# Kernel tuning notes

Hardware: AMD Instinct MI355X
Metric: run time of the kernel (lower is better)

The kernel has to match this reference:

```python
import jax, jax.numpy as jnp
import numpy as np

N_NODES = 100000
N_EDGES = 1600000
MSG_DIM = 16
HID_DIM = 16
N_ETYPE = 16
N_CLASSES = 64


def setup_inputs() -> dict:
    key = jax.random.key(0)
    ks = jax.random.split(key, 11)
    s = 1.0 / np.sqrt(HID_DIM)
    return {
        "features": jax.random.normal(ks[0], (N_NODES, HID_DIM), dtype=jnp.float32),
        "src": jax.random.randint(ks[1], (N_EDGES,), 0, N_NODES, dtype=jnp.int32),
        "dst": jax.random.randint(ks[2], (N_EDGES,), 0, N_NODES, dtype=jnp.int32),
        "e_type": jax.random.randint(ks[3], (N_EDGES,), 0, N_ETYPE, dtype=jnp.int32),
        "edge_emb": jax.random.normal(ks[4], (N_ETYPE, MSG_DIM * HID_DIM), dtype=jnp.float32),
        "W_ih": jax.random.uniform(ks[5], (3 * HID_DIM, MSG_DIM), dtype=jnp.float32, minval=-s, maxval=s),
        "W_hh": jax.random.uniform(ks[6], (3 * HID_DIM, HID_DIM), dtype=jnp.float32, minval=-s, maxval=s),
        "b_ih": jax.random.uniform(ks[7], (3 * HID_DIM,), dtype=jnp.float32, minval=-s, maxval=s),
        "b_hh": jax.random.uniform(ks[8], (3 * HID_DIM,), dtype=jnp.float32, minval=-s, maxval=s),
        "W_out": jax.random.normal(ks[9], (N_CLASSES, HID_DIM), dtype=jnp.float32) * s,
        "b_out": jax.random.normal(ks[10], (N_CLASSES,), dtype=jnp.float32) * 0.01,
    }


def reference(features, src, dst, e_type, edge_emb, W_ih, W_hh, b_ih, b_hh, W_out, b_out):
    # Per-edge message: A_e @ h_src, A_e = edge-type embedding reshaped [msg, hid]
    A = edge_emb[e_type].reshape(-1, MSG_DIM, HID_DIM)          # [E, M, H]
    msg = jnp.einsum("emh,eh->em", A, features[src])            # [E, M]
    # Sum-aggregate messages into destination nodes
    m = jax.ops.segment_sum(msg, dst, num_segments=N_NODES)     # [N, M]
    # Single-step GRU (PyTorch gate order: r, z, n)
    gx = m @ W_ih.T + b_ih                                      # [N, 3H]
    gh = features @ W_hh.T + b_hh                               # [N, 3H]
    xr, xz, xn = jnp.split(gx, 3, axis=-1)
    hr, hz, hn = jnp.split(gh, 3, axis=-1)
    r = jax.nn.sigmoid(xr + hr)
    z = jax.nn.sigmoid(xz + hz)
    n = jnp.tanh(xn + r * hn)
    h = (1.0 - z) * n + z * features                            # [N, H]
    return h @ W_out.T + b_out                                  # [N, C]
```

## Files before the change

### kernel.cpp

```cpp
#include <hip/hip_runtime.h>

#define NNODES 100000
#define NEDGES 1600000
#define HID 16
#define MSG 16
#define NTYPE 16
#define NCLS 64

__device__ __forceinline__ float sigmoid_f(float x) {
    return 1.0f / (1.0f + __expf(-x));
}

__device__ __forceinline__ float tanh_f(float x) {
    x = fminf(fmaxf(x, -15.0f), 15.0f);
    float e = __expf(2.0f * x);
    return (e - 1.0f) / (e + 1.0f);
}

__global__ __launch_bounds__(256) void ggnn_edge(
    const float* __restrict__ feat,
    const int* __restrict__ src,
    const int* __restrict__ dst,
    const int* __restrict__ etype,
    const float* __restrict__ edge_emb,
    float* __restrict__ magg)
{
    __shared__ float At[NTYPE * MSG * HID];
    for (int idx = threadIdx.x; idx < NTYPE * MSG * HID; idx += 256) {
        int t   = idx >> 8;
        int rem = idx & 255;
        int i   = rem >> 4;
        int hh  = rem & 15;
        At[(t << 8) | (hh << 4) | i] = edge_emb[idx];
    }
    __syncthreads();

    const long long total = (long long)NEDGES * MSG;
    for (long long w = (long long)blockIdx.x * 256 + threadIdx.x; w < total;
         w += (long long)gridDim.x * 256) {
        const int e = (int)(w >> 4);
        const int i = (int)(w & 15);
        const int s = src[e];
        const int d = dst[e];
        const int t = etype[e];

        const float4* fp = (const float4*)(feat + (size_t)s * HID);
        const float4 f0 = fp[0];
        const float4 f1 = fp[1];
        const float4 f2 = fp[2];
        const float4 f3 = fp[3];

        const float* a = At + (t << 8) + i;
        float acc;
        acc  = a[0*16]*f0.x + a[1*16]*f0.y + a[2*16]*f0.z + a[3*16]*f0.w;
        acc += a[4*16]*f1.x + a[5*16]*f1.y + a[6*16]*f1.z + a[7*16]*f1.w;
        acc += a[8*16]*f2.x + a[9*16]*f2.y + a[10*16]*f2.z + a[11*16]*f2.w;
        acc += a[12*16]*f3.x + a[13*16]*f3.y + a[14*16]*f3.z + a[15*16]*f3.w;

        atomicAdd(magg + (size_t)d * MSG + i, acc);
    }
}

__global__ __launch_bounds__(256) void ggnn_node(
    const float* __restrict__ feat,
    const float* __restrict__ magg,
    const float* __restrict__ W_ih,
    const float* __restrict__ W_hh,
    const float* __restrict__ b_ih,
    const float* __restrict__ b_hh,
    const float* __restrict__ W_out,
    const float* __restrict__ b_out,
    float* __restrict__ out)
{
    const int n = blockIdx.x * 256 + threadIdx.x;
    if (n >= NNODES) return;

    float hv[HID], mv[MSG];
    {
        const float4* hp = (const float4*)(feat + (size_t)n * HID);
        const float4* mp = (const float4*)(magg + (size_t)n * MSG);
        #pragma unroll
        for (int q = 0; q < 4; q++) {
            float4 a = hp[q];
            hv[4*q+0] = a.x; hv[4*q+1] = a.y; hv[4*q+2] = a.z; hv[4*q+3] = a.w;
            float4 b = mp[q];
            mv[4*q+0] = b.x; mv[4*q+1] = b.y; mv[4*q+2] = b.z; mv[4*q+3] = b.w;
        }
    }

    float hnew[HID];
    #pragma unroll
    for (int i = 0; i < HID; i++) {
        float xr = b_ih[i], xz = b_ih[16 + i], xn = b_ih[32 + i];
        float hr = b_hh[i], hz = b_hh[16 + i], hn = b_hh[32 + i];
        #pragma unroll
        for (int j = 0; j < HID; j++) {
            xr += W_ih[(i)      * 16 + j] * mv[j];
            xz += W_ih[(16 + i) * 16 + j] * mv[j];
            xn += W_ih[(32 + i) * 16 + j] * mv[j];
            hr += W_hh[(i)      * 16 + j] * hv[j];
            hz += W_hh[(16 + i) * 16 + j] * hv[j];
            hn += W_hh[(32 + i) * 16 + j] * hv[j];
        }
        float r  = sigmoid_f(xr + hr);
        float z  = sigmoid_f(xz + hz);
        float nn = tanh_f(xn + r * hn);
        hnew[i] = (1.0f - z) * nn + z * hv[i];
    }

    float4* op = (float4*)(out + (size_t)n * NCLS);
    #pragma unroll
    for (int c4 = 0; c4 < NCLS / 4; c4++) {
        float a0 = b_out[4*c4+0], a1 = b_out[4*c4+1], a2 = b_out[4*c4+2], a3 = b_out[4*c4+3];
        #pragma unroll
        for (int j = 0; j < HID; j++) {
            a0 += W_out[(4*c4+0) * 16 + j] * hnew[j];
            a1 += W_out[(4*c4+1) * 16 + j] * hnew[j];
            a2 += W_out[(4*c4+2) * 16 + j] * hnew[j];
            a3 += W_out[(4*c4+3) * 16 + j] * hnew[j];
        }
        float4 o; o.x = a0; o.y = a1; o.z = a2; o.w = a3;
        op[c4] = o;
    }
}

extern "C" void kernel_launch(void* const* d_in, const int* in_sizes, int n_in,
                              void* d_out, int out_size, void* d_ws, size_t ws_size,
                              hipStream_t stream) {
    const float* feat     = (const float*)d_in[0];
    const int*   src      = (const int*)d_in[1];
    const int*   dst      = (const int*)d_in[2];
    const int*   etype    = (const int*)d_in[3];
    const float* edge_emb = (const float*)d_in[4];
    const float* W_ih     = (const float*)d_in[5];
    const float* W_hh     = (const float*)d_in[6];
    const float* b_ih     = (const float*)d_in[7];
    const float* b_hh     = (const float*)d_in[8];
    const float* W_out    = (const float*)d_in[9];
    const float* b_out    = (const float*)d_in[10];
    float* out  = (float*)d_out;
    float* magg = (float*)d_ws;

    hipMemsetAsync(magg, 0, (size_t)NNODES * MSG * sizeof(float), stream);
    ggnn_edge<<<2560, 256, 0, stream>>>(feat, src, dst, etype, edge_emb, magg);
    ggnn_node<<<(NNODES + 255) / 256, 256, 0, stream>>>(
        feat, magg, W_ih, W_hh, b_ih, b_hh, W_out, b_out, out);
}
```

Baseline: 145.8 us.

## Build CSR by destination each call and aggregate messages without float atomics

Result: slower. 321.5 us (+120.5%).

```diff
diff --git a/kernel.cpp b/kernel.cpp
--- a/kernel.cpp
+++ b/kernel.cpp
@@ -7,6 +7,10 @@
 #define NTYPE 16
 #define NCLS 64
 
+#define SCAN_CHUNK 1024
+#define NB_SCAN ((NNODES + SCAN_CHUNK - 1) / SCAN_CHUNK)
+#define TSTRIDE 257
+
 __device__ __forceinline__ float sigmoid_f(float x) {
     return 1.0f / (1.0f + __expf(-x));
 }
@@ -15,6 +19,135 @@
     x = fminf(fmaxf(x, -15.0f), 15.0f);
     float e = __expf(2.0f * x);
     return (e - 1.0f) / (e + 1.0f);
+}
+
+__global__ __launch_bounds__(256) void hist_k(const int* __restrict__ dst,
+                                              int* __restrict__ cnt) {
+    int e = blockIdx.x * 256 + threadIdx.x;
+    if (e < NEDGES) atomicAdd(&cnt[dst[e]], 1);
+}
+
+__global__ __launch_bounds__(256) void scan_bsum(const int* __restrict__ cnt,
+                                                 int* __restrict__ bsum) {
+    int base = blockIdx.x * SCAN_CHUNK + threadIdx.x * 4;
+    int s = 0;
+    #pragma unroll
+    for (int q = 0; q < 4; q++) {
+        int idx = base + q;
+        if (idx < NNODES) s += cnt[idx];
+    }
+    #pragma unroll
+    for (int d = 32; d > 0; d >>= 1) s += __shfl_down(s, d, 64);
+    __shared__ int ws[4];
+    int lane = threadIdx.x & 63, wid = threadIdx.x >> 6;
+    if (lane == 0) ws[wid] = s;
+    __syncthreads();
+    if (threadIdx.x == 0) bsum[blockIdx.x] = ws[0] + ws[1] + ws[2] + ws[3];
+}
+
+__global__ __launch_bounds__(128) void scan_top(int* __restrict__ bsum,
+                                                int* __restrict__ rowptr) {
+    int t = threadIdx.x;
+    int v = (t < NB_SCAN) ? bsum[t] : 0;
+    int lane = t & 63, wid = t >> 6;
+    int s = v;
+    #pragma unroll
+    for (int d = 1; d < 64; d <<= 1) {
+        int u = __shfl_up(s, d, 64);
+        if (lane >= d) s += u;
+    }
+    __shared__ int wtot[2];
+    if (lane == 63) wtot[wid] = s;
+    __syncthreads();
+    int excl = s - v + (wid == 1 ? wtot[0] : 0);
+    if (t < NB_SCAN) bsum[t] = excl;
+    if (t == 0) rowptr[NNODES] = NEDGES;
+}
+
+__global__ __launch_bounds__(256) void scan_write(const int* __restrict__ bsum,
+                                                  int* __restrict__ cntpos,
+                                                  int* __restrict__ rowptr) {
+    int t = threadIdx.x;
+    int base = blockIdx.x * SCAN_CHUNK + t * 4;
+    int v[4];
+    int ts = 0;
+    #pragma unroll
+    for (int q = 0; q < 4; q++) {
+        int idx = base + q;
+        v[q] = (idx < NNODES) ? cntpos[idx] : 0;
+        ts += v[q];
+    }
+    int s = ts;
+    int lane = t & 63, wid = t >> 6;
+    #pragma unroll
+    for (int d = 1; d < 64; d <<= 1) {
+        int u = __shfl_up(s, d, 64);
+        if (lane >= d) s += u;
+    }
+    __shared__ int wsum[4];
+    if (lane == 63) wsum[wid] = s;
+    __syncthreads();
+    int wbase = 0;
+    for (int w = 0; w < wid; w++) wbase += wsum[w];
+    int off = bsum[blockIdx.x] + wbase + (s - ts);
+    #pragma unroll
+    for (int q = 0; q < 4; q++) {
+        int idx = base + q;
+        if (idx < NNODES) {
+            rowptr[idx] = off;
+            cntpos[idx] = off;
+        }
+        off += v[q];
+    }
+}
+
+__global__ __launch_bounds__(256) void scatter_k(const int* __restrict__ src,
+                                                 const int* __restrict__ dst,
+                                                 const int* __restrict__ et,
+                                                 int* __restrict__ pos,
+                                                 int* __restrict__ rec) {
+    int e = blockIdx.x * 256 + threadIdx.x;
+    if (e < NEDGES) {
+        int d = dst[e];
+        int p = atomicAdd(&pos[d], 1);
+        rec[p] = src[e] | (et[e] << 17);
+    }
+}
+
+__global__ __launch_bounds__(256) void agg_k(const float* __restrict__ feat,
+                                             const int* __restrict__ rowptr,
+                                             const int* __restrict__ rec,
+                                             const float* __restrict__ edge_emb,
+                                             float* __restrict__ magg) {
+    __shared__ float At[NTYPE * TSTRIDE];
+    for (int idx = threadIdx.x; idx < NTYPE * MSG * HID; idx += 256) {
+        int t   = idx >> 8;
+        int rem = idx & 255;
+        int i   = rem >> 4;
+        int h   = rem & 15;
+        At[t * TSTRIDE + h * 16 + i] = edge_emb[idx];
+    }
+    __syncthreads();
+
+    int node = blockIdx.x * 16 + (threadIdx.x >> 4);
+    int i = threadIdx.x & 15;
+    if (node >= NNODES) return;
+
+    int jb = rowptr[node], je = rowptr[node + 1];
+    float acc = 0.0f;
+    for (int j = jb; j < je; j++) {
+        int r = rec[j];
+        int s = r & 0x1FFFF;
+        int t = r >> 17;
+        const float4* fp = (const float4*)(feat + (size_t)s * HID);
+        float4 f0 = fp[0], f1 = fp[1], f2 = fp[2], f3 = fp[3];
+        const float* a = At + t * TSTRIDE + i;
+        acc += a[0*16]*f0.x + a[1*16]*f0.y + a[2*16]*f0.z + a[3*16]*f0.w;
+        acc += a[4*16]*f1.x + a[5*16]*f1.y + a[6*16]*f1.z + a[7*16]*f1.w;
+        acc += a[8*16]*f2.x + a[9*16]*f2.y + a[10*16]*f2.z + a[11*16]*f2.w;
+        acc += a[12*16]*f3.x + a[13*16]*f3.y + a[14*16]*f3.z + a[15*16]*f3.w;
+    }
+    magg[(size_t)node * MSG + i] = acc;
 }
 
 __global__ __launch_bounds__(256) void ggnn_edge(
@@ -27,14 +160,10 @@
 {
     __shared__ float At[NTYPE * MSG * HID];
     for (int idx = threadIdx.x; idx < NTYPE * MSG * HID; idx += 256) {
-        int t   = idx >> 8;
-        int rem = idx & 255;
-        int i   = rem >> 4;
-        int hh  = rem & 15;
+        int t = idx >> 8, rem = idx & 255, i = rem >> 4, hh = rem & 15;
         At[(t << 8) | (hh << 4) | i] = edge_emb[idx];
     }
     __syncthreads();
-
     const long long total = (long long)NEDGES * MSG;
     for (long long w = (long long)blockIdx.x * 256 + threadIdx.x; w < total;
          w += (long long)gridDim.x * 256) {
@@ -43,20 +172,14 @@
         const int s = src[e];
         const int d = dst[e];
         const int t = etype[e];
-
         const float4* fp = (const float4*)(feat + (size_t)s * HID);
-        const float4 f0 = fp[0];
-        const float4 f1 = fp[1];
-        const float4 f2 = fp[2];
-        const float4 f3 = fp[3];
-
+        const float4 f0 = fp[0], f1 = fp[1], f2 = fp[2], f3 = fp[3];
         const float* a = At + (t << 8) + i;
         float acc;
         acc  = a[0*16]*f0.x + a[1*16]*f0.y + a[2*16]*f0.z + a[3*16]*f0.w;
         acc += a[4*16]*f1.x + a[5*16]*f1.y + a[6*16]*f1.z + a[7*16]*f1.w;
         acc += a[8*16]*f2.x + a[9*16]*f2.y + a[10*16]*f2.z + a[11*16]*f2.w;
         acc += a[12*16]*f3.x + a[13*16]*f3.y + a[14*16]*f3.z + a[15*16]*f3.w;
-
         atomicAdd(magg + (size_t)d * MSG + i, acc);
     }
 }
@@ -138,11 +261,27 @@
     const float* b_hh     = (const float*)d_in[8];
     const float* W_out    = (const float*)d_in[9];
     const float* b_out    = (const float*)d_in[10];
-    float* out  = (float*)d_out;
-    float* magg = (float*)d_ws;
-
-    hipMemsetAsync(magg, 0, (size_t)NNODES * MSG * sizeof(float), stream);
-    ggnn_edge<<<2560, 256, 0, stream>>>(feat, src, dst, etype, edge_emb, magg);
+    float* out = (float*)d_out;
+
+    float* magg   = (float*)d_ws;
+    int*   rowptr = (int*)d_ws + NNODES * MSG;
+    int*   cntpos = rowptr + (NNODES + 1);
+    int*   bsum   = cntpos + NNODES;
+    int*   rec    = bsum + 128;
+    size_t need   = ((size_t)NNODES * MSG + (NNODES + 1) + NNODES + 128 + NEDGES) * 4;
+
+    if (ws_size >= need) {
+        hipMemsetAsync(cntpos, 0, (size_t)NNODES * sizeof(int), stream);
+        hist_k    <<<(NEDGES + 255) / 256, 256, 0, stream>>>(dst, cntpos);
+        scan_bsum <<<NB_SCAN, 256, 0, stream>>>(cntpos, bsum);
+        scan_top  <<<1, 128, 0, stream>>>(bsum, rowptr);
+        scan_write<<<NB_SCAN, 256, 0, stream>>>(bsum, cntpos, rowptr);
+        scatter_k <<<(NEDGES + 255) / 256, 256, 0, stream>>>(src, dst, etype, cntpos, rec);
+        agg_k     <<<NNODES / 16, 256, 0, stream>>>(feat, rowptr, rec, edge_emb, magg);
+    } else {
+        hipMemsetAsync(magg, 0, (size_t)NNODES * MSG * sizeof(float), stream);
+        ggnn_edge<<<2560, 256, 0, stream>>>(feat, src, dst, etype, edge_emb, magg);
+    }
     ggnn_node<<<(NNODES + 255) / 256, 256, 0, stream>>>(
         feat, magg, W_ih, W_hh, b_ih, b_hh, W_out, b_out, out);
 }
```

## Bucket edges by destination block and aggregate in shared memory

Applied to the files above, without the earlier changes.

Result: slower. 303.3 us (+108.0%).

```diff
diff --git a/kernel.cpp b/kernel.cpp
--- a/kernel.cpp
+++ b/kernel.cpp
@@ -7,14 +7,196 @@
 #define NTYPE 16
 #define NCLS 64
 
+#define CHSZ 4096
+#define NCH ((NEDGES + CHSZ - 1) / CHSZ)
+#define NBK ((NNODES + 255) / 256)
+#define M_SCAN (NBK * NCH)
+#define SCH 1024
+#define NSB ((M_SCAN + SCH - 1) / SCH)
+
 __device__ __forceinline__ float sigmoid_f(float x) {
     return 1.0f / (1.0f + __expf(-x));
 }
-
 __device__ __forceinline__ float tanh_f(float x) {
     x = fminf(fmaxf(x, -15.0f), 15.0f);
     float e = __expf(2.0f * x);
     return (e - 1.0f) / (e + 1.0f);
+}
+
+__global__ __launch_bounds__(256) void hist_k(const int* __restrict__ dst,
+                                              int* __restrict__ cntmat) {
+    __shared__ int cnt[NBK];
+    const int t = threadIdx.x, ch = blockIdx.x;
+    for (int b = t; b < NBK; b += 256) cnt[b] = 0;
+    __syncthreads();
+    #pragma unroll
+    for (int k = 0; k < CHSZ / 256; k++) {
+        int e = ch * CHSZ + k * 256 + t;
+        if (e < NEDGES) atomicAdd(&cnt[dst[e] >> 8], 1);
+    }
+    __syncthreads();
+    for (int b = t; b < NBK; b += 256) cntmat[b * NCH + ch] = cnt[b];
+}
+
+__global__ __launch_bounds__(256) void scan_bsum(const int* __restrict__ x,
+                                                 int* __restrict__ bsum) {
+    const int t = threadIdx.x;
+    int base = blockIdx.x * SCH + t * 4;
+    int s = 0;
+    #pragma unroll
+    for (int q = 0; q < 4; q++) {
+        int idx = base + q;
+        if (idx < M_SCAN) s += x[idx];
+    }
+    #pragma unroll
+    for (int d = 32; d > 0; d >>= 1) s += __shfl_down(s, d, 64);
+    __shared__ int ws[4];
+    int lane = t & 63, w = t >> 6;
+    if (lane == 0) ws[w] = s;
+    __syncthreads();
+    if (t == 0) bsum[blockIdx.x] = ws[0] + ws[1] + ws[2] + ws[3];
+}
+
+__global__ __launch_bounds__(256) void scan_top(int* __restrict__ bsum) {
+    const int t = threadIdx.x;
+    int v = (t < NSB) ? bsum[t] : 0;
+    int lane = t & 63, w = t >> 6;
+    int s = v;
+    #pragma unroll
+    for (int d = 1; d < 64; d <<= 1) {
+        int u = __shfl_up(s, d, 64);
+        if (lane >= d) s += u;
+    }
+    __shared__ int ws[4];
+    if (lane == 63) ws[w] = s;
+    __syncthreads();
+    int base = 0;
+    #pragma unroll
+    for (int q = 0; q < 4; q++) if (q < w) base += ws[q];
+    if (t < NSB) bsum[t] = base + s - v;
+}
+
+__global__ __launch_bounds__(256) void scan_write(const int* __restrict__ bsum,
+                                                  int* __restrict__ x) {
+    const int t = threadIdx.x;
+    int base = blockIdx.x * SCH + t * 4;
+    int v[4]; int ts = 0;
+    #pragma unroll
+    for (int q = 0; q < 4; q++) {
+        int idx = base + q;
+        v[q] = (idx < M_SCAN) ? x[idx] : 0;
+        ts += v[q];
+    }
+    int lane = t & 63, w = t >> 6;
+    int s = ts;
+    #pragma unroll
+    for (int d = 1; d < 64; d <<= 1) {
+        int u = __shfl_up(s, d, 64);
+        if (lane >= d) s += u;
+    }
+    __shared__ int ws[4];
+    if (lane == 63) ws[w] = s;
+    __syncthreads();
+    int wbase = 0;
+    #pragma unroll
+    for (int q = 0; q < 4; q++) if (q < w) wbase += ws[q];
+    int run = bsum[blockIdx.x] + wbase + (s - ts);
+    #pragma unroll
+    for (int q = 0; q < 4; q++) {
+        int idx = base + q;
+        if (idx < M_SCAN) x[idx] = run;
+        run += v[q];
+    }
+}
+
+__global__ __launch_bounds__(256) void scatter_k(const int* __restrict__ src,
+                                                 const int* __restrict__ dst,
+                                                 const int* __restrict__ et,
+                                                 const int* __restrict__ offmat,
+                                                 int* __restrict__ rec) {
+    __shared__ int offc[NBK];
+    const int t = threadIdx.x, ch = blockIdx.x;
+    for (int b = t; b < NBK; b += 256) offc[b] = offmat[b * NCH + ch];
+    __syncthreads();
+    #pragma unroll
+    for (int k = 0; k < CHSZ / 256; k++) {
+        int e = ch * CHSZ + k * 256 + t;
+        if (e < NEDGES) {
+            int d = dst[e];
+            int b = d >> 8;
+            int pos = atomicAdd(&offc[b], 1);
+            rec[pos] = src[e] | (et[e] << 17) | ((d & 255) << 21);
+        }
+    }
+}
+
+__global__ __launch_bounds__(256) void agg_k(const float* __restrict__ feat,
+                                             const int* __restrict__ offmat,
+                                             const int* __restrict__ rec,
+                                             const float* __restrict__ edge_emb,
+                                             float* __restrict__ magg) {
+    __shared__ float At[NTYPE * 257];
+    __shared__ float acc[256 * 17];
+    const int t = threadIdx.x, b = blockIdx.x;
+
+    for (int idx = t; idx < NTYPE * MSG * HID; idx += 256) {
+        int ty  = idx >> 8;
+        int rem = idx & 255;
+        int i   = rem >> 4;
+        int h   = rem & 15;
+        At[ty * 257 + h * 16 + i] = edge_emb[idx];
+    }
+    for (int k = t; k < 256 * 17; k += 256) acc[k] = 0.0f;
+    __syncthreads();
+
+    const int jb = offmat[b * NCH];
+    const int je = (b == NBK - 1) ? NEDGES : offmat[(b + 1) * NCH];
+    const int g = t >> 4, i = t & 15;
+
+    int j = jb + g;
+    for (; j + 16 < je; j += 32) {
+        int r0 = rec[j], r1 = rec[j + 16];
+        int s0 = r0 & 0x1FFFF, ty0 = (r0 >> 17) & 15, ld0 = r0 >> 21;
+        int s1 = r1 & 0x1FFFF, ty1 = (r1 >> 17) & 15, ld1 = r1 >> 21;
+        const float4* fp0 = (const float4*)(feat + (size_t)s0 * HID);
+        const float4* fp1 = (const float4*)(feat + (size_t)s1 * HID);
+        float4 a0 = fp0[0], a1 = fp0[1], a2 = fp0[2], a3 = fp0[3];
+        float4 c0 = fp1[0], c1 = fp1[1], c2 = fp1[2], c3 = fp1[3];
+        const float* pa = At + ty0 * 257 + i;
+        const float* pb = At + ty1 * 257 + i;
+        float m0, m1;
+        m0  = pa[0*16]*a0.x + pa[1*16]*a0.y + pa[2*16]*a0.z + pa[3*16]*a0.w;
+        m0 += pa[4*16]*a1.x + pa[5*16]*a1.y + pa[6*16]*a1.z + pa[7*16]*a1.w;
+        m0 += pa[8*16]*a2.x + pa[9*16]*a2.y + pa[10*16]*a2.z + pa[11*16]*a2.w;
+        m0 += pa[12*16]*a3.x + pa[13*16]*a3.y + pa[14*16]*a3.z + pa[15*16]*a3.w;
+        m1  = pb[0*16]*c0.x + pb[1*16]*c0.y + pb[2*16]*c0.z + pb[3*16]*c0.w;
+        m1 += pb[4*16]*c1.x + pb[5*16]*c1.y + pb[6*16]*c1.z + pb[7*16]*c1.w;
+        m1 += pb[8*16]*c2.x + pb[9*16]*c2.y + pb[10*16]*c2.z + pb[11*16]*c2.w;
+        m1 += pb[12*16]*c3.x + pb[13*16]*c3.y + pb[14*16]*c3.z + pb[15*16]*c3.w;
+        atomicAdd(&acc[ld0 * 17 + i], m0);
+        atomicAdd(&acc[ld1 * 17 + i], m1);
+    }
+    if (j < je) {
+        int r0 = rec[j];
+        int s0 = r0 & 0x1FFFF, ty0 = (r0 >> 17) & 15, ld0 = r0 >> 21;
+        const float4* fp0 = (const float4*)(feat + (size_t)s0 * HID);
+        float4 a0 = fp0[0], a1 = fp0[1], a2 = fp0[2], a3 = fp0[3];
+        const float* pa = At + ty0 * 257 + i;
+        float m0;
+        m0  = pa[0*16]*a0.x + pa[1*16]*a0.y + pa[2*16]*a0.z + pa[3*16]*a0.w;
+        m0 += pa[4*16]*a1.x + pa[5*16]*a1.y + pa[6*16]*a1.z + pa[7*16]*a1.w;
+        m0 += pa[8*16]*a2.x + pa[9*16]*a2.y + pa[10*16]*a2.z + pa[11*16]*a2.w;
+        m0 += pa[12*16]*a3.x + pa[13*16]*a3.y + pa[14*16]*a3.z + pa[15*16]*a3.w;
+        atomicAdd(&acc[ld0 * 17 + i], m0);
+    }
+    __syncthreads();
+
+    const int nb = b * 256;
+    for (int k = t; k < 256 * 16; k += 256) {
+        int ln = k >> 4, ii = k & 15;
+        int n = nb + ln;
+        if (n < NNODES) magg[(size_t)n * MSG + ii] = acc[ln * 17 + ii];
+    }
 }
 
 __global__ __launch_bounds__(256) void ggnn_edge(
@@ -27,14 +209,10 @@
 {
     __shared__ float At[NTYPE * MSG * HID];
     for (int idx = threadIdx.x; idx < NTYPE * MSG * HID; idx += 256) {
-        int t   = idx >> 8;
-        int rem = idx & 255;
-        int i   = rem >> 4;
-        int hh  = rem & 15;
-        At[(t << 8) | (hh << 4) | i] = edge_emb[idx];
-    }
-    __syncthreads();
-
+        int ty = idx >> 8, rem = idx & 255, i = rem >> 4, hh = rem & 15;
+        At[(ty << 8) | (hh << 4) | i] = edge_emb[idx];
+    }
+    __syncthreads();
     const long long total = (long long)NEDGES * MSG;
     for (long long w = (long long)blockIdx.x * 256 + threadIdx.x; w < total;
          w += (long long)gridDim.x * 256) {
@@ -42,26 +220,20 @@
         const int i = (int)(w & 15);
         const int s = src[e];
         const int d = dst[e];
-        const int t = etype[e];
-
+        const int ty = etype[e];
         const float4* fp = (const float4*)(feat + (size_t)s * HID);
-        const float4 f0 = fp[0];
-        const float4 f1 = fp[1];
-        const float4 f2 = fp[2];
-        const float4 f3 = fp[3];
-
-        const float* a = At + (t << 8) + i;
-        float acc;
-        acc  = a[0*16]*f0.x + a[1*16]*f0.y + a[2*16]*f0.z + a[3*16]*f0.w;
-        acc += a[4*16]*f1.x + a[5*16]*f1.y + a[6*16]*f1.z + a[7*16]*f1.w;
-        acc += a[8*16]*f2.x + a[9*16]*f2.y + a[10*16]*f2.z + a[11*16]*f2.w;
-        acc += a[12*16]*f3.x + a[13*16]*f3.y + a[14*16]*f3.z + a[15*16]*f3.w;
-
-        atomicAdd(magg + (size_t)d * MSG + i, acc);
-    }
-}
-
-__global__ __launch_bounds__(256) void ggnn_node(
+        const float4 f0 = fp[0], f1 = fp[1], f2 = fp[2], f3 = fp[3];
+        const float* a = At + (ty << 8) + i;
+        float m;
+        m  = a[0*16]*f0.x + a[1*16]*f0.y + a[2*16]*f0.z + a[3*16]*f0.w;
+        m += a[4*16]*f1.x + a[5*16]*f1.y + a[6*16]*f1.z + a[7*16]*f1.w;
+        m += a[8*16]*f2.x + a[9*16]*f2.y + a[10*16]*f2.z + a[11*16]*f2.w;
+        m += a[12*16]*f3.x + a[13*16]*f3.y + a[14*16]*f3.z + a[15*16]*f3.w;
+        atomicAdd(magg + (size_t)d * MSG + i, m);
+    }
+}
+
+__global__ __launch_bounds__(256) void node_k(
     const float* __restrict__ feat,
     const float* __restrict__ magg,
     const float* __restrict__ W_ih,
@@ -72,55 +244,69 @@
     const float* __restrict__ b_out,
     float* __restrict__ out)
 {
-    const int n = blockIdx.x * 256 + threadIdx.x;
-    if (n >= NNODES) return;
-
-    float hv[HID], mv[MSG];
-    {
+    __shared__ float hn_s[256 * 20];
+    __shared__ float Wo_s[NCLS * 17];
+    __shared__ float bo_s[NCLS];
+
+    const int t = threadIdx.x;
+    for (int k = t; k < NCLS * 16; k += 256) Wo_s[(k >> 4) * 17 + (k & 15)] = W_out[k];
+    if (t < NCLS) bo_s[t] = b_out[t];
+
+    const int n = blockIdx.x * 256 + t;
+    if (n < NNODES) {
+        float hv[HID], mv[MSG];
         const float4* hp = (const float4*)(feat + (size_t)n * HID);
         const float4* mp = (const float4*)(magg + (size_t)n * MSG);
         #pragma unroll
         for (int q = 0; q < 4; q++) {
             float4 a = hp[q];
             hv[4*q+0] = a.x; hv[4*q+1] = a.y; hv[4*q+2] = a.z; hv[4*q+3] = a.w;
-            float4 b = mp[q];
-            mv[4*q+0] = b.x; mv[4*q+1] = b.y; mv[4*q+2] = b.z; mv[4*q+3] = b.w;
+            float4 c = mp[q];
+            mv[4*q+0] = c.x; mv[4*q+1] = c.y; mv[4*q+2] = c.z; mv[4*q+3] = c.w;
         }
-    }
-
-    float hnew[HID];
-    #pragma unroll
-    for (int i = 0; i < HID; i++) {
-        float xr = b_ih[i], xz = b_ih[16 + i], xn = b_ih[32 + i];
-        float hr = b_hh[i], hz = b_hh[16 + i], hn = b_hh[32 + i];
         #pragma unroll
-        for (int j = 0; j < HID; j++) {
-            xr += W_ih[(i)      * 16 + j] * mv[j];
-            xz += W_ih[(16 + i) * 16 + j] * mv[j];
-            xn += W_ih[(32 + i) * 16 + j] * mv[j];
-            hr += W_hh[(i)      * 16 + j] * hv[j];
-            hz += W_hh[(16 + i) * 16 + j] * hv[j];
-            hn += W_hh[(32 + i) * 16 + j] * hv[j];
+        for (int i = 0; i < HID; i++) {
+            float xr = b_ih[i], xz = b_ih[16 + i], xn = b_ih[32 + i];
+            float hr = b_hh[i], hz = b_hh[16 + i], hn = b_hh[32 + i];
+            #pragma unroll
+            for (int j = 0; j < HID; j++) {
+                xr += W_ih[(i)      * 16 + j] * mv[j];
+                xz += W_ih[(16 + i) * 16 + j] * mv[j];
+                xn += W_ih[(32 + i) * 16 + j] * mv[j];
+                hr += W_hh[(i)      * 16 + j] * hv[j];
+                hz += W_hh[(16 + i) * 16 + j] * hv[j];
+                hn += W_hh[(32 + i) * 16 + j] * hv[j];
+            }
+            float r  = sigmoid_f(xr + hr);
+            float z  = sigmoid_f(xz + hz);
+            float nn = tanh_f(xn + r * hn);
+            hn_s[t * 20 + i] = (1.0f - z) * nn + z * hv[i];
         }
-        float r  = sigmoid_f(xr + hr);
-        float z  = sigmoid_f(xz + hz);
-        float nn = tanh_f(xn + r * hn);
-        hnew[i] = (1.0f - z) * nn + z * hv[i];
-    }
-
-    float4* op = (float4*)(out + (size_t)n * NCLS);
-    #pragma unroll
-    for (int c4 = 0; c4 < NCLS / 4; c4++) {
-        float a0 = b_out[4*c4+0], a1 = b_out[4*c4+1], a2 = b_out[4*c4+2], a3 = b_out[4*c4+3];
-        #pragma unroll
-        for (int j = 0; j < HID; j++) {
-            a0 += W_out[(4*c4+0) * 16 + j] * hnew[j];
-            a1 += W_out[(4*c4+1) * 16 + j] * hnew[j];
-            a2 += W_out[(4*c4+2) * 16 + j] * hnew[j];
-            a3 += W_out[(4*c4+3) * 16 + j] * hnew[j];
+    }
+    __syncthreads();
+
+    const int c = t & 63;
+    float wr[16];
+    #pragma unroll
+    for (int j = 0; j < 16; j++) wr[j] = Wo_s[c * 17 + j];
+    const float bo = bo_s[c];
+    const int nb = blockIdx.x * 256;
+
+    #pragma unroll 4
+    for (int it = 0; it < 64; it++) {
+        int k = t + 256 * it;
+        int ln = k >> 6;
+        int n2 = nb + ln;
+        if (n2 < NNODES) {
+            const float4* hq = (const float4*)(hn_s + ln * 20);
+            float4 h0 = hq[0], h1 = hq[1], h2 = hq[2], h3 = hq[3];
+            float a = bo;
+            a += wr[0]*h0.x + wr[1]*h0.y + wr[2]*h0.z + wr[3]*h0.w;
+            a += wr[4]*h1.x + wr[5]*h1.y + wr[6]*h1.z + wr[7]*h1.w;
+            a += wr[8]*h2.x + wr[9]*h2.y + wr[10]*h2.z + wr[11]*h2.w;
+            a += wr[12]*h3.x + wr[13]*h3.y + wr[14]*h3.z + wr[15]*h3.w;
+            out[(size_t)n2 * NCLS + c] = a;
         }
-        float4 o; o.x = a0; o.y = a1; o.z = a2; o.w = a3;
-        op[c4] = o;
     }
 }
 
@@ -138,11 +324,25 @@
     const float* b_hh     = (const float*)d_in[8];
     const float* W_out    = (const float*)d_in[9];
     const float* b_out    = (const float*)d_in[10];
-    float* out  = (float*)d_out;
-    float* magg = (float*)d_ws;
-
-    hipMemsetAsync(magg, 0, (size_t)NNODES * MSG * sizeof(float), stream);
-    ggnn_edge<<<2560, 256, 0, stream>>>(feat, src, dst, etype, edge_emb, magg);
-    ggnn_node<<<(NNODES + 255) / 256, 256, 0, stream>>>(
+    float* out = (float*)d_out;
+
+    float* magg   = (float*)d_ws;
+    int*   offmat = (int*)d_ws + (size_t)NNODES * MSG;
+    int*   bsum   = offmat + M_SCAN;
+    int*   rec    = bsum + 256;
+    size_t need   = ((size_t)NNODES * MSG + M_SCAN + 256 + NEDGES) * 4;
+
+    if (ws_size >= need) {
+        hist_k    <<<NCH, 256, 0, stream>>>(dst, offmat);
+        scan_bsum <<<NSB, 256, 0, stream>>>(offmat, bsum);
+        scan_top  <<<1, 256, 0, stream>>>(bsum);
+        scan_write<<<NSB, 256, 0, stream>>>(bsum, offmat);
+        scatter_k <<<NCH, 256, 0, stream>>>(src, dst, etype, offmat, rec);
+        agg_k     <<<NBK, 256, 0, stream>>>(feat, offmat, rec, edge_emb, magg);
+    } else {
+        hipMemsetAsync(magg, 0, (size_t)NNODES * MSG * sizeof(float), stream);
+        ggnn_edge<<<2560, 256, 0, stream>>>(feat, src, dst, etype, edge_emb, magg);
+    }
+    node_k<<<(NNODES + 255) / 256, 256, 0, stream>>>(
         feat, magg, W_ih, W_hh, b_ih, b_hh, W_out, b_out, out);
 }
```
